# Kernel tuning notes

Measured on AMD Instinct MI355X. Metric: run time of the kernel, lower is better.

Reference implementation:

```python
import jax, jax.numpy as jnp
import numpy as np

N, D_IN, D_OUT, K = 8192, 64, 128, 16


def setup_inputs() -> dict:
    key = jax.random.key(0)
    k1, k2, k3 = jax.random.split(key, 3)
    x = jax.random.normal(k1, (N, D_IN), dtype=jnp.float32)
    W1 = jax.random.normal(k2, (2 * D_IN, D_OUT), dtype=jnp.float32) * 0.05
    b1 = jnp.zeros((D_OUT,), dtype=jnp.float32)
    W2 = jax.random.normal(k3, (D_OUT, D_OUT), dtype=jnp.float32) * 0.05
    b2 = jnp.zeros((D_OUT,), dtype=jnp.float32)
    return {"x": x, "W1": W1, "b1": b1, "W2": W2, "b2": b2, "k": K}


def reference(x, W1, b1, W2, b2, k):
    # dynamic kNN graph (PyG knn(x, x, k) includes self as nearest neighbor)
    sq = jnp.sum(x * x, axis=-1)                      # [N]
    dist = sq[:, None] + sq[None, :] - 2.0 * (x @ x.T)  # [N, N] squared dists
    _, idx = jax.lax.top_k(-dist, k)                  # [N, k] nearest indices
    x_j = x[idx]                                      # [N, k, D_IN] gather
    x_i = jnp.broadcast_to(x[:, None, :], x_j.shape)  # [N, k, D_IN]
    e = jnp.concatenate([x_i, x_j - x_i], axis=-1)    # [N, k, 2*D_IN]
    h = jax.nn.relu(e @ W1 + b1) @ W2 + b2            # [N, k, D_OUT]
    return jnp.mean(h, axis=1)                        # mean aggregation -> [N, D_OUT]
```

## Files before the change

### kernel.cpp

```cpp
#include <hip/hip_runtime.h>

#define N 8192
#define DIN 64
#define DOUT 128
#define KNN 16
#define MSAMP 1024
#define NBX 16
#define NST 8
#define CAND_R 64
#define CAND_C (NBX * CAND_R)
#define EPS 1.0f
#define DELTA_Q 64
#define VCAP 128

typedef unsigned long long u64;
typedef __attribute__((ext_vector_type(8))) short bf16x8;
typedef __attribute__((ext_vector_type(4))) float floatx4;

__device__ __forceinline__ unsigned mono(float f) {
    unsigned u = __float_as_uint(f);
    return (u & 0x80000000u) ? ~u : (u | 0x80000000u);
}
__device__ __forceinline__ unsigned short f2bf(float f) {
    unsigned u = __float_as_uint(f);
    return (unsigned short)((u + 0x7FFFu + ((u >> 16) & 1u)) >> 16);
}
__device__ __forceinline__ unsigned qdist(float dist) {
    int q = (int)(dist * 128.0f) + 2;
    q = max(q, 0); return (unsigned)min(q, 65535);
}

__global__ __launch_bounds__(256, 4) void k_pre(const float* __restrict__ x,
                                                const float* __restrict__ W1,
                                                const float* __restrict__ b1,
                                                float* __restrict__ sq,
                                                float* __restrict__ sqs,
                                                unsigned short* __restrict__ Xh,
                                                unsigned short* __restrict__ Xs,
                                                float* __restrict__ U,
                                                float* __restrict__ V) {
    __shared__ float xs[8][DIN];
    int t = threadIdx.x;
    int r0 = blockIdx.x * 8;
    if (t < 128) {
        float4 xv = ((const float4*)x)[(size_t)r0 * (DIN / 4) + t];
        ((float4*)xs)[t] = xv;
        ushort4 h4;
        h4.x = f2bf(xv.x); h4.y = f2bf(xv.y);
        h4.z = f2bf(xv.z); h4.w = f2bf(xv.w);
        *(ushort4*)&Xh[r0 * DIN + t * 4] = h4;
    }
    __syncthreads();
    if (t < 16) {
        const float* xr = xs[0];
        ushort4 h4;
        h4.x = f2bf(xr[t * 4 + 0]); h4.y = f2bf(xr[t * 4 + 1]);
        h4.z = f2bf(xr[t * 4 + 2]); h4.w = f2bf(xr[t * 4 + 3]);
        *(ushort4*)&Xs[(size_t)blockIdx.x * DIN + t * 4] = h4;
    }
    if (t < 8) {
        const float4* xr = (const float4*)xs[t];
        float s0 = 0.f, s1 = 0.f, s2 = 0.f, s3 = 0.f;
#pragma unroll
        for (int q = 0; q < DIN / 4; ++q) {
            float4 a = xr[q];
            s0 = fmaf(a.x, a.x, s0); s1 = fmaf(a.y, a.y, s1);
            s2 = fmaf(a.z, a.z, s2); s3 = fmaf(a.w, a.w, s3);
        }
        float sv = (s0 + s1) + (s2 + s3);
        sq[r0 + t] = sv;
        if (t == 0) sqs[blockIdx.x] = sv;
    }
    int o = t & 127, g = t >> 7;
    float aU[4], aV[4];
#pragma unroll
    for (int u = 0; u < 4; ++u) { aU[u] = 0.f; aV[u] = 0.f; }
    for (int kk = 0; kk < DIN; ++kk) {
        float whi = W1[kk * DOUT + o];
        float wlo = W1[(DIN + kk) * DOUT + o];
        float wd = whi - wlo;
#pragma unroll
        for (int u = 0; u < 4; ++u) {
            float xvv = xs[g * 4 + u][kk];
            aU[u] = fmaf(xvv, wd, aU[u]);
            aV[u] = fmaf(xvv, wlo, aV[u]);
        }
    }
    float bb = b1[o];
#pragma unroll
    for (int u = 0; u < 4; ++u) {
        int r = r0 + g * 4 + u;
        U[(size_t)r * DOUT + o] = aU[u] + bb;
        V[(size_t)r * DOUT + o] = aV[u];
    }
}

__global__ __launch_bounds__(1024, 4) void k_pretau(const unsigned short* __restrict__ Xh,
                                                    const unsigned short* __restrict__ Xs,
                                                    const float* __restrict__ sq,
                                                    const float* __restrict__ sqs,
                                                    float* __restrict__ tauf) {
    __shared__ __align__(16) unsigned short qls[16 * MSAMP];
    int tid = threadIdx.x, w = tid >> 6, l = tid & 63;
    int m = l & 15, quad = l >> 4, ko = quad * 8;
    int rt = blockIdx.x;
    int irow = rt * 16 + m;
    size_t arow = (size_t)irow * DIN;
    bf16x8 iH0 = *(const bf16x8*)(Xh + arow + ko);
    bf16x8 iH1 = *(const bf16x8*)(Xh + arow + 32 + ko);
    float si = sq[irow];
    int swz = (m & 7) << 4;
    for (int it = 0; it < 4; ++it) {
        int s16 = w * 64 + it * 16;
        const unsigned short* sp = Xs + (size_t)(s16 + m) * DIN;
        bf16x8 sH0 = *(const bf16x8*)(sp + ko);
        bf16x8 sH1 = *(const bf16x8*)(sp + 32 + ko);
        floatx4 acc = {0.f, 0.f, 0.f, 0.f};
        acc = __builtin_amdgcn_mfma_f32_16x16x32_bf16(sH0, iH0, acc, 0, 0, 0);
        acc = __builtin_amdgcn_mfma_f32_16x16x32_bf16(sH1, iH1, acc, 0, 0, 0);
        int sc0 = s16 + quad * 4;
        float4 sj = *(const float4*)(sqs + sc0);
        unsigned q0 = qdist(fmaf(-2.0f, acc[0], si + sj.x));
        unsigned q1 = qdist(fmaf(-2.0f, acc[1], si + sj.y));
        unsigned q2 = qdist(fmaf(-2.0f, acc[2], si + sj.z));
        unsigned q3 = qdist(fmaf(-2.0f, acc[3], si + sj.w));
        u64 pk = (u64)q0 | ((u64)q1 << 16) | ((u64)q2 << 32) | ((u64)q3 << 48);
        *(u64*)&qls[m * MSAMP + (sc0 ^ swz)] = pk;
    }
    __syncthreads();
    const uint4* qv = (const uint4*)qls;
    unsigned v[16];
#pragma unroll
    for (int k = 0; k < 2; ++k) {
        uint4 t4 = qv[w * 128 + k * 64 + l];
        v[k*8+0] = t4.x & 0xFFFFu; v[k*8+1] = t4.x >> 16;
        v[k*8+2] = t4.y & 0xFFFFu; v[k*8+3] = t4.y >> 16;
        v[k*8+4] = t4.z & 0xFFFFu; v[k*8+5] = t4.z >> 16;
        v[k*8+6] = t4.w & 0xFFFFu; v[k*8+7] = t4.w >> 16;
    }
#pragma unroll
    for (int i = 0; i < 16; ++i)
        asm volatile("" : "+v"(v[i]));
    unsigned p = 0;
#pragma unroll
    for (int b = 13; b >= 0; --b) {
        unsigned c16 = p | (1u << b);
        int a0 = 0, a1 = 0, a2 = 0, a3 = 0;
#pragma unroll
        for (int i = 0; i < 4; ++i) {
            a0 += (int)(v[i]      - c16) >> 31;
            a1 += (int)(v[4 + i]  - c16) >> 31;
            a2 += (int)(v[8 + i]  - c16) >> 31;
            a3 += (int)(v[12 + i] - c16) >> 31;
        }
        int neg = (a0 + a1) + (a2 + a3);
#pragma unroll
        for (int mk = 1; mk < 64; mk <<= 1)
            neg += __shfl_xor(neg, mk);
        if (-neg < 16) p = c16;
    }
    if (l == 0) tauf[rt * 16 + w] = (float)p * (1.0f / 128.0f);
}

__global__ __launch_bounds__(256, 8) void k_main(const unsigned short* __restrict__ Xh,
                                                 const float* __restrict__ sq,
                                                 const float* __restrict__ tauf,
                                                 unsigned* __restrict__ cand,
                                                 unsigned* __restrict__ cntpart) {
    __shared__ __align__(16) short ldsH[64 * 72];
    int tid = threadIdx.x, w = tid >> 6, l = tid & 63;
    int m = l & 15, ko = (l >> 4) * 8;
    int bx = blockIdx.x;
    int rt = blockIdx.y * 4 + w;
    size_t arow = (size_t)(rt * 16 + m) * DIN;
    bf16x8 aH0 = *(const bf16x8*)(Xh + arow + ko);
    bf16x8 aH1 = *(const bf16x8*)(Xh + arow + 32 + ko);
    int rg[4]; float T[4]; float si[4]; int rowcnt[4];
#pragma unroll
    for (int reg = 0; reg < 4; ++reg) {
        rg[reg] = rt * 16 + (l >> 4) * 4 + reg;
        si[reg] = sq[rg[reg]];
        T[reg] = tauf[rg[reg]] + EPS - si[reg];
        rowcnt[reg] = 0;
    }
    int qs = l & 48;
    unsigned lmask = (1u << (l & 15)) - 1u;
    int srw = tid >> 3, scol8 = (tid & 7) * 8;

    for (int st = 0; st < NST; ++st) {
        int jbase = bx * (NST * 64) + st * 64;
        __syncthreads();
        *(bf16x8*)&ldsH[srw * 72 + scol8] =
            *(const bf16x8*)(Xh + (size_t)(jbase + srw) * DIN + scol8);
        *(bf16x8*)&ldsH[(srw + 32) * 72 + scol8] =
            *(const bf16x8*)(Xh + (size_t)(jbase + srw + 32) * DIN + scol8);
        __syncthreads();
#pragma unroll
        for (int it = 0; it < 4; ++it) {
            int br = it * 16 + m;
            bf16x8 bH0 = *(const bf16x8*)&ldsH[br * 72 + ko];
            bf16x8 bH1 = *(const bf16x8*)&ldsH[br * 72 + 32 + ko];
            floatx4 acc = {0.f, 0.f, 0.f, 0.f};
            acc = __builtin_amdgcn_mfma_f32_16x16x32_bf16(aH0, bH0, acc, 0, 0, 0);
            acc = __builtin_amdgcn_mfma_f32_16x16x32_bf16(aH1, bH1, acc, 0, 0, 0);
            int jcol = jbase + it * 16 + m;
            float sqj = sq[jcol];
#pragma unroll
            for (int reg = 0; reg < 4; ++reg) {
                float tv = fmaf(-2.0f, acc[reg], sqj);
                bool pass = tv <= T[reg];
                u64 bal = __ballot(pass);
                if (bal) {
                    unsigned m16 = (unsigned)((bal >> qs) & 0xFFFFull);
                    if (pass) {
                        int slot = rowcnt[reg] + __popc(m16 & lmask);
                        if (slot < CAND_R)
                            cand[(size_t)rg[reg] * CAND_C + bx * CAND_R + slot] =
                                (qdist(tv + si[reg]) << 16) | (unsigned)jcol;
                    }
                    rowcnt[reg] += __popc(m16);
                }
            }
        }
    }
    if ((l & 15) == 0) {
#pragma unroll
        for (int reg = 0; reg < 4; ++reg)
            cntpart[rg[reg] * NBX + bx] = (unsigned)min(rowcnt[reg], CAND_R);
    }
}

__global__ __launch_bounds__(256, 8) void k_post(
    const float* __restrict__ x, const float* __restrict__ sq,
    const unsigned* __restrict__ cntpart, const unsigned* __restrict__ cand,
    const float* __restrict__ U, const float* __restrict__ V,
    const float* __restrict__ W2, const float* __restrict__ b2,
    float* __restrict__ out)
{
    __shared__ union {
        struct { unsigned short vlist[4][VCAP];
                 u64 ekeys[4][VCAP]; } e;
        struct { float ag[4][DOUT];
                 float w2t[32 * DOUT]; } a;
    } sm;
    __shared__ int knn_s[4][KNN];
    int t = threadIdx.x;
    int w = t >> 6, l = t & 63;
    int row = blockIdx.x * 4 + w;
    {
        unsigned c[NBX];
        const unsigned* cp = cntpart + (size_t)row * NBX;
#pragma unroll
        for (int b = 0; b < NBX; ++b) c[b] = min(cp[b], (unsigned)CAND_R);
        const unsigned* crow = cand + (size_t)row * CAND_C;
        unsigned qq[NBX], kk[NBX];
#pragma unroll
        for (int u = 0; u < NBX; ++u) {
            unsigned kv = crow[u * 64 + l];
            kk[u] = kv;
            qq[u] = ((unsigned)l < c[u]) ? (kv >> 16) : 0xFFFFFFFFu;
        }
        unsigned p = 0;
#pragma unroll
        for (int b = 13; b >= 0; --b) {
            unsigned c16 = p | (1u << b);
            int cnt = 0;
#pragma unroll
            for (int u = 0; u < NBX; ++u)
                cnt += __popcll(__ballot(qq[u] < c16));
            if (cnt < 16) p = c16;
        }
        unsigned thr = p + DELTA_Q;
        int nv = 0;
        u64 lm = (l == 63) ? 0xFFFFFFFFFFFFFFFFull >> 1 : (1ull << l) - 1ull;
#pragma unroll
        for (int u = 0; u < NBX; ++u) {
            bool pred = qq[u] <= thr;
            u64 bal = __ballot(pred);
            int slot = nv + __popcll(bal & lm);
            if (pred && slot < VCAP)
                sm.e.vlist[w][slot] = (unsigned short)(kk[u] & 0xFFFFu);
            nv += __popcll(bal);
        }
        nv = min(nv, VCAP);
        __syncthreads();
        float sqi = sq[row];
        const float* xi = x + (size_t)row * DIN;
#pragma unroll
        for (int r = 0; r < VCAP / 64; ++r) {
            int v = l + 64 * r;
            if (v < nv) {
                int j = (int)sm.e.vlist[w][v];
                const float4* bj = (const float4*)(x + (size_t)j * DIN);
                float s0 = 0.f, s1 = 0.f, s2 = 0.f, s3 = 0.f;
                float4 rb[8];
#pragma unroll
                for (int q = 0; q < 8; ++q) rb[q] = bj[q];
#pragma unroll
                for (int q = 0; q < 8; ++q) {
                    s0 = fmaf(xi[4 * q + 0], rb[q].x, s0);
                    s1 = fmaf(xi[4 * q + 1], rb[q].y, s1);
                    s2 = fmaf(xi[4 * q + 2], rb[q].z, s2);
                    s3 = fmaf(xi[4 * q + 3], rb[q].w, s3);
                }
#pragma unroll
                for (int q = 0; q < 8; ++q) rb[q] = bj[8 + q];
#pragma unroll
                for (int q = 0; q < 8; ++q) {
                    s0 = fmaf(xi[32 + 4 * q + 0], rb[q].x, s0);
                    s1 = fmaf(xi[32 + 4 * q + 1], rb[q].y, s1);
                    s2 = fmaf(xi[32 + 4 * q + 2], rb[q].z, s2);
                    s3 = fmaf(xi[32 + 4 * q + 3], rb[q].w, s3);
                }
                float d = (s0 + s1) + (s2 + s3);
                float dist = fmaf(-2.0f, d, sqi + sq[j]);
                sm.e.ekeys[w][v] = ((u64)mono(dist) << 32) | (unsigned)j;
            }
        }
#pragma unroll
        for (int r = 0; r < VCAP / 64; ++r) {
            int v = l + 64 * r;
            if (v < nv) {
                u64 mykey = sm.e.ekeys[w][v];
                int rank = 0;
                for (int i = 0; i < nv; ++i)
                    rank += (sm.e.ekeys[w][i] < mykey) ? 1 : 0;
                if (rank < KNN)
                    knn_s[w][rank] = (int)(unsigned)(mykey & 0xFFFFFFFFull);
            }
        }
    }
    __syncthreads();
    {
        int o = t & 127, g = t >> 7;
        int row0 = blockIdx.x * 4;
#pragma unroll
        for (int r = 0; r < 2; ++r) {
            int rr = g * 2 + r;
            int i = row0 + rr;
            float u = U[(size_t)i * DOUT + o];
            float acc = 0.f;
#pragma unroll
            for (int q = 0; q < KNN; ++q)
                acc += fmaxf(u + V[(size_t)knn_s[rr][q] * DOUT + o], 0.0f);
            sm.a.ag[rr][o] = acc * (1.0f / KNN);
        }
        float a2[2] = {0.f, 0.f};
#pragma unroll
        for (int tile = 0; tile < 4; ++tile) {
            __syncthreads();
#pragma unroll
            for (int u = 0; u < 4; ++u)
                ((float4*)sm.a.w2t)[t + u * 256] =
                    ((const float4*)(W2 + tile * 32 * DOUT))[t + u * 256];
            __syncthreads();
#pragma unroll
            for (int q4 = 0; q4 < 8; ++q4) {
                int kb = tile * 32 + q4 * 4;
                float4 a0 = *(const float4*)&sm.a.ag[g * 2 + 0][kb];
                float4 a1 = *(const float4*)&sm.a.ag[g * 2 + 1][kb];
                float w0 = sm.a.w2t[(q4 * 4 + 0) * DOUT + o - tile * 32 * DOUT + tile * 32 * DOUT];
                w0 = sm.a.w2t[(q4 * 4 + 0) * DOUT + o];
                float w1 = sm.a.w2t[(q4 * 4 + 1) * DOUT + o];
                float w2v = sm.a.w2t[(q4 * 4 + 2) * DOUT + o];
                float w3 = sm.a.w2t[(q4 * 4 + 3) * DOUT + o];
                a2[0] = fmaf(a0.x, w0, a2[0]);  a2[1] = fmaf(a1.x, w0, a2[1]);
                a2[0] = fmaf(a0.y, w1, a2[0]);  a2[1] = fmaf(a1.y, w1, a2[1]);
                a2[0] = fmaf(a0.z, w2v, a2[0]); a2[1] = fmaf(a1.z, w2v, a2[1]);
                a2[0] = fmaf(a0.w, w3, a2[0]);  a2[1] = fmaf(a1.w, w3, a2[1]);
            }
        }
        float bb = b2[o];
#pragma unroll
        for (int r = 0; r < 2; ++r)
            out[(size_t)(row0 + g * 2 + r) * DOUT + o] = a2[r] + bb;
    }
}

extern "C" void kernel_launch(void* const* d_in, const int* in_sizes, int n_in,
                              void* d_out, int out_size, void* d_ws, size_t ws_size,
                              hipStream_t stream) {
    const float* x  = (const float*)d_in[0];
    const float* W1 = (const float*)d_in[1];
    const float* b1 = (const float*)d_in[2];
    const float* W2 = (const float*)d_in[3];
    const float* b2 = (const float*)d_in[4];
    float* out = (float*)d_out;

    char* ws = (char*)d_ws;
    float*          sq      = (float*)(ws);
    float*          sqs     = (float*)(ws + 32768);
    float*          tauf    = (float*)(ws + 40960);
    unsigned short* Xs      = (unsigned short*)(ws + 73728);
    unsigned short* Xh      = (unsigned short*)(ws + 655360);
    float*          U       = (float*)(ws + 2097152);
    float*          V       = (float*)(ws + 6291456);
    unsigned*       cntpart = (unsigned*)(ws + 10485760);
    unsigned*       cand    = (unsigned*)(ws + 11534336);

    k_pre<<<N / 8, 256, 0, stream>>>(x, W1, b1, sq, sqs, Xh, Xs, U, V);
    k_pretau<<<N / 16, 1024, 0, stream>>>(Xh, Xs, sq, sqs, tauf);
    k_main<<<dim3(NBX, 128), 256, 0, stream>>>(Xh, sq, tauf, cand, cntpart);
    k_post<<<N / 4, 256, 0, stream>>>(x, sq, cntpart, cand, U, V, W2, b2, out);
}
```

Before: 157.1 us.

## Double-buffer LDS tiles in k_main and skip radix select when candidates fit

In k_main the shared X tile becomes two buffers. The next 64-row tile is loaded into registers while MFMAs run on the current one, then written to the other buffer, which removes one barrier per stage. In k_post the 14-step ballot radix-select for the threshold is skipped when a row's total candidate count fits in VCAP, and all candidates are kept instead. It also unrolls the W1 loop in the precompute kernel and removes a redundant shared load. The cost is double the LDS footprint and more live registers, which could affect occupancy.

Result: slower. 180.4 us (+14.8%).

```diff
diff --git a/kernel.cpp b/kernel.cpp
--- a/kernel.cpp
+++ b/kernel.cpp
@@ -75,9 +75,12 @@
     float aU[4], aV[4];
 #pragma unroll
     for (int u = 0; u < 4; ++u) { aU[u] = 0.f; aV[u] = 0.f; }
+    const float* Whi = W1 + o;
+    const float* Wlo = W1 + DIN * DOUT + o;
+#pragma unroll 8
     for (int kk = 0; kk < DIN; ++kk) {
-        float whi = W1[kk * DOUT + o];
-        float wlo = W1[(DIN + kk) * DOUT + o];
+        float whi = Whi[kk * DOUT];
+        float wlo = Wlo[kk * DOUT];
         float wd = whi - wlo;
 #pragma unroll
         for (int u = 0; u < 4; ++u) {
@@ -167,7 +170,7 @@
                                                  const float* __restrict__ tauf,
                                                  unsigned* __restrict__ cand,
                                                  unsigned* __restrict__ cntpart) {
-    __shared__ __align__(16) short ldsH[64 * 72];
+    __shared__ __align__(16) short ldsH[2][64 * 72];
     int tid = threadIdx.x, w = tid >> 6, l = tid & 63;
     int m = l & 15, ko = (l >> 4) * 8;
     int bx = blockIdx.x;
@@ -187,19 +190,27 @@
     unsigned lmask = (1u << (l & 15)) - 1u;
     int srw = tid >> 3, scol8 = (tid & 7) * 8;
 
+    int jb0 = bx * (NST * 64);
+    *(bf16x8*)&ldsH[0][srw * 72 + scol8] =
+        *(const bf16x8*)(Xh + (size_t)(jb0 + srw) * DIN + scol8);
+    *(bf16x8*)&ldsH[0][(srw + 32) * 72 + scol8] =
+        *(const bf16x8*)(Xh + (size_t)(jb0 + 32 + srw) * DIN + scol8);
+    __syncthreads();
+
     for (int st = 0; st < NST; ++st) {
-        int jbase = bx * (NST * 64) + st * 64;
-        __syncthreads();
-        *(bf16x8*)&ldsH[srw * 72 + scol8] =
-            *(const bf16x8*)(Xh + (size_t)(jbase + srw) * DIN + scol8);
-        *(bf16x8*)&ldsH[(srw + 32) * 72 + scol8] =
-            *(const bf16x8*)(Xh + (size_t)(jbase + srw + 32) * DIN + scol8);
-        __syncthreads();
+        int cur = st & 1;
+        int jbase = jb0 + st * 64;
+        bf16x8 n0, n1;
+        if (st < NST - 1) {
+            int jn = jbase + 64;
+            n0 = *(const bf16x8*)(Xh + (size_t)(jn + srw) * DIN + scol8);
+            n1 = *(const bf16x8*)(Xh + (size_t)(jn + 32 + srw) * DIN + scol8);
+        }
 #pragma unroll
         for (int it = 0; it < 4; ++it) {
             int br = it * 16 + m;
-            bf16x8 bH0 = *(const bf16x8*)&ldsH[br * 72 + ko];
-            bf16x8 bH1 = *(const bf16x8*)&ldsH[br * 72 + 32 + ko];
+            bf16x8 bH0 = *(const bf16x8*)&ldsH[cur][br * 72 + ko];
+            bf16x8 bH1 = *(const bf16x8*)&ldsH[cur][br * 72 + 32 + ko];
             floatx4 acc = {0.f, 0.f, 0.f, 0.f};
             acc = __builtin_amdgcn_mfma_f32_16x16x32_bf16(aH0, bH0, acc, 0, 0, 0);
             acc = __builtin_amdgcn_mfma_f32_16x16x32_bf16(aH1, bH1, acc, 0, 0, 0);
@@ -222,6 +233,11 @@
                 }
             }
         }
+        if (st < NST - 1) {
+            *(bf16x8*)&ldsH[cur ^ 1][srw * 72 + scol8] = n0;
+            *(bf16x8*)&ldsH[cur ^ 1][(srw + 32) * 72 + scol8] = n1;
+        }
+        __syncthreads();
     }
     if ((l & 15) == 0) {
 #pragma unroll
@@ -249,9 +265,13 @@
     int row = blockIdx.x * 4 + w;
     {
         unsigned c[NBX];
+        int total = 0;
         const unsigned* cp = cntpart + (size_t)row * NBX;
 #pragma unroll
-        for (int b = 0; b < NBX; ++b) c[b] = min(cp[b], (unsigned)CAND_R);
+        for (int b = 0; b < NBX; ++b) {
+            c[b] = min(cp[b], (unsigned)CAND_R);
+            total += (int)c[b];
+        }
         const unsigned* crow = cand + (size_t)row * CAND_C;
         unsigned qq[NBX], kk[NBX];
 #pragma unroll
@@ -260,17 +280,22 @@
             kk[u] = kv;
             qq[u] = ((unsigned)l < c[u]) ? (kv >> 16) : 0xFFFFFFFFu;
         }
-        unsigned p = 0;
-#pragma unroll
-        for (int b = 13; b >= 0; --b) {
-            unsigned c16 = p | (1u << b);
-            int cnt = 0;
-#pragma unroll
-            for (int u = 0; u < NBX; ++u)
-                cnt += __popcll(__ballot(qq[u] < c16));
-            if (cnt < 16) p = c16;
-        }
-        unsigned thr = p + DELTA_Q;
+        unsigned thr;
+        if (total > VCAP) {
+            unsigned p = 0;
+#pragma unroll
+            for (int b = 13; b >= 0; --b) {
+                unsigned c16 = p | (1u << b);
+                int cnt = 0;
+#pragma unroll
+                for (int u = 0; u < NBX; ++u)
+                    cnt += __popcll(__ballot(qq[u] < c16));
+                if (cnt < 16) p = c16;
+            }
+            thr = p + DELTA_Q;
+        } else {
+            thr = 0xFFFFFFFEu;
+        }
         int nv = 0;
         u64 lm = (l == 63) ? 0xFFFFFFFFFFFFFFFFull >> 1 : (1ull << l) - 1ull;
 #pragma unroll
@@ -359,8 +384,7 @@
                 int kb = tile * 32 + q4 * 4;
                 float4 a0 = *(const float4*)&sm.a.ag[g * 2 + 0][kb];
                 float4 a1 = *(const float4*)&sm.a.ag[g * 2 + 1][kb];
-                float w0 = sm.a.w2t[(q4 * 4 + 0) * DOUT + o - tile * 32 * DOUT + tile * 32 * DOUT];
-                w0 = sm.a.w2t[(q4 * 4 + 0) * DOUT + o];
+                float w0 = sm.a.w2t[(q4 * 4 + 0) * DOUT + o];
                 float w1 = sm.a.w2t[(q4 * 4 + 1) * DOUT + o];
                 float w2v = sm.a.w2t[(q4 * 4 + 2) * DOUT + o];
                 float w3 = sm.a.w2t[(q4 * 4 + 3) * DOUT + o];
```
